# Optimization experiments

Hardware: AMD Instinct MI355X
Metric: run time of the kernel (lower is better)

The kernel has to match this reference:

```python
import jax, jax.numpy as jnp
import numpy as np

VAR0, VAR1 = 0.1, 0.2      # cfg['variance']
THR = 0.5                   # overlap_thresh
NEGPOS_RATIO = 3


def point_form(p):  # center form [P,4] -> corner form
    return jnp.concatenate([p[:, :2] - p[:, 2:] / 2, p[:, :2] + p[:, 2:] / 2], axis=1)


def iou(a, b):  # a [N,4], b [P,4], both corner form -> [N,P]
    lt = jnp.maximum(a[:, None, :2], b[None, :, :2])
    rb = jnp.minimum(a[:, None, 2:], b[None, :, 2:])
    wh = jnp.maximum(rb - lt, 0.0)
    inter = wh[..., 0] * wh[..., 1]
    area_a = (a[:, 2] - a[:, 0]) * (a[:, 3] - a[:, 1])
    area_b = (b[:, 2] - b[:, 0]) * (b[:, 3] - b[:, 1])
    return inter / (area_a[:, None] + area_b[None, :] - inter)


def encode(matched, priors):  # matched corner [P,4], priors center [P,4]
    g_cxcy = ((matched[:, :2] + matched[:, 2:]) / 2 - priors[:, :2]) / (VAR0 * priors[:, 2:])
    g_wh = jnp.log((matched[:, 2:] - matched[:, :2]) / priors[:, 2:]) / VAR1
    return jnp.concatenate([g_cxcy, g_wh], axis=1)


def match_one(truths, labels, priors):
    # truths [N,4] corner, labels [N] int, priors [P,4] center
    ov = iou(truths, point_form(priors))            # [N,P]
    best_prior_idx = jnp.argmax(ov, axis=1)         # [N] best prior per truth
    best_truth_overlap = jnp.max(ov, axis=0)        # [P]
    best_truth_idx = jnp.argmax(ov, axis=0)         # [P]
    # ensure every truth keeps its best prior
    best_truth_overlap = best_truth_overlap.at[best_prior_idx].set(2.0)
    best_truth_idx = best_truth_idx.at[best_prior_idx].set(jnp.arange(truths.shape[0]))
    matched = truths[best_truth_idx]                # [P,4]
    conf = jnp.where(best_truth_overlap < THR, 0, labels[best_truth_idx] + 1)  # bkg=0
    return encode(matched, priors), conf


def multibox_loss(loc_data, conf_data, priors, truths, labels):
    B, P, C = conf_data.shape
    loc_t, conf_t = jax.vmap(lambda t, l: match_one(t, l, priors))(truths, labels)
    loc_t = jax.lax.stop_gradient(loc_t)            # targets are detached
    pos = conf_t > 0                                # [B,P]

    # localization: masked smooth-L1 (beta=1), sum reduction
    d = loc_data - loc_t
    ad = jnp.abs(d)
    sl1 = jnp.where(ad < 1.0, 0.5 * d * d, ad - 0.5)
    loss_l = jnp.sum(sl1 * pos[..., None].astype(sl1.dtype))

    # hard negative mining: per-prior CE proxy, positives zeroed, double argsort rank
    lse = jax.nn.logsumexp(conf_data, axis=2)
    gathered = jnp.take_along_axis(conf_data, conf_t[..., None], axis=2)[..., 0]
    lc = jnp.where(pos, 0.0, lse - gathered)        # [B,P]
    loss_idx = jnp.argsort(-lc, axis=1)
    idx_rank = jnp.argsort(loss_idx, axis=1)
    num_pos = jnp.sum(pos, axis=1)                  # [B]
    num_neg = jnp.minimum(NEGPOS_RATIO * num_pos, P - 1)
    neg = idx_rank < num_neg[:, None]
    sel = pos | neg

    # confidence loss on pos + hard negatives, sum reduction
    logp = jax.nn.log_softmax(conf_data, axis=2)
    ce = -jnp.take_along_axis(logp, conf_t[..., None], axis=2)[..., 0]
    loss_c = jnp.sum(ce * sel.astype(ce.dtype))

    total = jnp.sum(num_pos).astype(loss_l.dtype)
    return loss_l / total, loss_c / total


def setup_inputs() -> dict:
    key = jax.random.key(0)
    kl, kc, kp, kt, ky = jax.random.split(key, 5)
    B, P, C, N = 64, 24564, 21, 16
    loc_data = 0.1 * jax.random.normal(kl, (B, P, 4), dtype=jnp.float32)
    conf_data = jax.random.normal(kc, (B, P, C), dtype=jnp.float32)
    pr = jax.random.uniform(kp, (P, 4), dtype=jnp.float32)
    priors = jnp.concatenate([pr[:, :2] * 0.9 + 0.05, pr[:, 2:] * 0.26 + 0.04], axis=1)
    pts = jax.random.uniform(kt, (B, N, 2, 2), dtype=jnp.float32) * 0.8 + 0.05
    truths = jnp.concatenate([jnp.min(pts, axis=2), jnp.max(pts, axis=2) + 0.02], axis=-1)
    labels = jax.random.randint(ky, (B, N), 0, 20, dtype=jnp.int32)
    return {"loc_data": loc_data, "conf_data": conf_data, "priors": priors,
            "truths": truths, "labels": labels}


def reference(loc_data, conf_data, priors, truths, labels):
    return multibox_loss(loc_data, conf_data, priors, truths, labels)
```

## Files before the change

kernel.cpp:

```cpp
#include <hip/hip_runtime.h>
#include <math.h>

constexpr int Bn = 64;
constexpr int Pn = 24564;
constexpr int Cn = 21;
constexpr int Nn = 16;
constexpr int CH = 12;
constexpr int CHSZ = 2048;
constexpr float VAR0 = 0.1f, VAR1 = 0.2f, THRv = 0.5f;

__device__ __forceinline__ float iou_tp(float tx1, float ty1, float tx2, float ty2,
                                        float px1, float py1, float px2, float py2) {
  float lx = fmaxf(tx1, px1), ly = fmaxf(ty1, py1);
  float rx = fminf(tx2, px2), ry = fminf(ty2, py2);
  float w = fmaxf(rx - lx, 0.f), h = fmaxf(ry - ly, 0.f);
  float inter = w * h;
  float aa = (tx2 - tx1) * (ty2 - ty1);
  float ab = (px2 - px1) * (py2 - py1);
  return __fdividef(inter, aa + ab - inter);
}

__global__ void best_prior_part(const float* __restrict__ priors,
                                const float* __restrict__ truths,
                                float* __restrict__ pbv, int* __restrict__ pbi) {
  const int c = blockIdx.x;
  const int b = blockIdx.y;
  const int tid = threadIdx.x;
  __shared__ float4 tru[Nn];
  if (tid < Nn) tru[tid] = reinterpret_cast<const float4*>(truths)[b * Nn + tid];
  __syncthreads();

  float bv[Nn];
  int bi[Nn];
#pragma unroll
  for (int n = 0; n < Nn; n++) { bv[n] = -1.0f; bi[n] = 0x7fffffff; }

  const int base = c * CHSZ;
#pragma unroll
  for (int j = 0; j < CHSZ / 256; j++) {
    int p = base + j * 256 + tid;
    if (p < Pn) {
      float4 pr = reinterpret_cast<const float4*>(priors)[p];
      float px1 = pr.x - pr.z * 0.5f, py1 = pr.y - pr.w * 0.5f;
      float px2 = pr.x + pr.z * 0.5f, py2 = pr.y + pr.w * 0.5f;
#pragma unroll
      for (int n = 0; n < Nn; n++) {
        float v = iou_tp(tru[n].x, tru[n].y, tru[n].z, tru[n].w, px1, py1, px2, py2);
        if (v > bv[n]) { bv[n] = v; bi[n] = p; }
      }
    }
  }

  const int lane = tid & 63, wv = tid >> 6;
  __shared__ float swv[4][Nn];
  __shared__ int swi[4][Nn];
#pragma unroll
  for (int n = 0; n < Nn; n++) {
    float v = bv[n]; int i = bi[n];
#pragma unroll
    for (int m = 1; m < 64; m <<= 1) {
      float ov = __shfl_xor(v, m, 64);
      int oi = __shfl_xor(i, m, 64);
      if (ov > v || (ov == v && oi < i)) { v = ov; i = oi; }
    }
    if (lane == 0) { swv[wv][n] = v; swi[wv][n] = i; }
  }
  __syncthreads();
  if (tid < Nn) {
    float v = swv[0][tid]; int i = swi[0][tid];
#pragma unroll
    for (int w = 1; w < 4; w++) {
      float ov = swv[w][tid]; int oi = swi[w][tid];
      if (ov > v || (ov == v && oi < i)) { v = ov; i = oi; }
    }
    pbv[(b * CH + c) * Nn + tid] = v;
    pbi[(b * CH + c) * Nn + tid] = i;
  }
}

__global__ void best_prior_merge(const float* __restrict__ pbv,
                                 const int* __restrict__ pbi,
                                 int* __restrict__ bpi) {
  const int b = blockIdx.x;
  const int n = threadIdx.x;
  if (n < Nn) {
    float v = pbv[(b * CH) * Nn + n];
    int i = pbi[(b * CH) * Nn + n];
#pragma unroll
    for (int c = 1; c < CH; c++) {
      float ov = pbv[(b * CH + c) * Nn + n];
      int oi = pbi[(b * CH + c) * Nn + n];
      if (ov > v || (ov == v && oi < i)) { v = ov; i = oi; }
    }
    bpi[b * Nn + n] = i;
  }
}

__global__ __launch_bounds__(256, 8) void match_loss_kernel(
    const float* __restrict__ loc,
    const float* __restrict__ conf,
    const float* __restrict__ priors,
    const float* __restrict__ truths,
    const int* __restrict__ labels,
    const int* __restrict__ bpi,
    float* __restrict__ lc_out,
    int* __restrict__ num_pos,
    float* __restrict__ acc ) {
  const int b = blockIdx.y;
  const int tid = threadIdx.x;
  const int wv = tid >> 6, lane = tid & 63;
  const int p = blockIdx.x * 256 + tid;

  __shared__ float4 tru[Nn];
  __shared__ int lab[Nn];
  __shared__ int bp[Nn];
  if (tid < Nn) {
    tru[tid] = reinterpret_cast<const float4*>(truths)[b * Nn + tid];
    lab[tid] = labels[b * Nn + tid];
    bp[tid]  = bpi[b * Nn + tid];
  }
  __syncthreads();

  float my_ll = 0.f, my_cep = 0.f;
  int my_np = 0;

  if (p < Pn) {
    const float* crow = conf + ((size_t)b * Pn + p) * Cn;
    float r[Cn];
#pragma unroll
    for (int c = 0; c < Cn; c++) r[c] = crow[c];

    float4 pr = reinterpret_cast<const float4*>(priors)[p];
    float px1 = pr.x - pr.z * 0.5f, py1 = pr.y - pr.w * 0.5f;
    float px2 = pr.x + pr.z * 0.5f, py2 = pr.y + pr.w * 0.5f;

    float best = -1.0f;
    int bidx = 0;
#pragma unroll
    for (int n = 0; n < Nn; n++) {
      float v = iou_tp(tru[n].x, tru[n].y, tru[n].z, tru[n].w, px1, py1, px2, py2);
      if (v > best) { best = v; bidx = n; }
    }
#pragma unroll
    for (int n = 0; n < Nn; n++) {
      if (bp[n] == p) { best = 2.0f; bidx = n; }
    }

    int conf_t = (best < THRv) ? 0 : (lab[bidx] + 1);
    bool pos = conf_t > 0;

    float s = 0.f;
#pragma unroll
    for (int c = 0; c < Cn; c++) s += __expf(r[c]);
    float lse = __logf(s);
    float ce = lse - crow[conf_t];

    lc_out[(size_t)b * Pn + p] = pos ? 0.f : ce;

    if (pos) {
      my_np = 1;
      my_cep = ce;
      float4 t = tru[bidx];
      float gx = ((t.x + t.z) * 0.5f - pr.x) / (VAR0 * pr.z);
      float gy = ((t.y + t.w) * 0.5f - pr.y) / (VAR0 * pr.w);
      float gw = __logf((t.z - t.x) / pr.z) / VAR1;
      float gh = __logf((t.w - t.y) / pr.w) / VAR1;
      const float* lrow = loc + ((size_t)b * Pn + p) * 4;
      float d0 = lrow[0] - gx, d1 = lrow[1] - gy, d2 = lrow[2] - gw, d3 = lrow[3] - gh;
      float a0 = fabsf(d0), a1 = fabsf(d1), a2 = fabsf(d2), a3 = fabsf(d3);
      my_ll  = (a0 < 1.f ? 0.5f * d0 * d0 : a0 - 0.5f);
      my_ll += (a1 < 1.f ? 0.5f * d1 * d1 : a1 - 0.5f);
      my_ll += (a2 < 1.f ? 0.5f * d2 * d2 : a2 - 0.5f);
      my_ll += (a3 < 1.f ? 0.5f * d3 * d3 : a3 - 0.5f);
    }
  }

  float ll = my_ll, cep = my_cep;
  int np = my_np;
#pragma unroll
  for (int m2 = 1; m2 < 64; m2 <<= 1) {
    ll  += __shfl_xor(ll, m2, 64);
    cep += __shfl_xor(cep, m2, 64);
    np  += __shfl_xor(np, m2, 64);
  }
  __shared__ float sw_ll[4], sw_ce[4];
  __shared__ int sw_np[4];
  if (lane == 0) { sw_ll[wv] = ll; sw_ce[wv] = cep; sw_np[wv] = np; }
  __syncthreads();
  if (tid == 0) {
    float tll = sw_ll[0] + sw_ll[1] + sw_ll[2] + sw_ll[3];
    float tce = sw_ce[0] + sw_ce[1] + sw_ce[2] + sw_ce[3];
    int tnp = sw_np[0] + sw_np[1] + sw_np[2] + sw_np[3];
    if (tll != 0.f) atomicAdd(&acc[0], tll);
    if (tce != 0.f) atomicAdd(&acc[1], tce);
    if (tnp != 0)   atomicAdd(&num_pos[b], tnp);
  }
}

__global__ __launch_bounds__(1024) void topk_kernel(const float* __restrict__ lc,
                                                    const int* __restrict__ num_pos,
                                                    float* __restrict__ topk) {
  const int b = blockIdx.x;
  const int tid = threadIdx.x;
  const int wv = tid >> 6, lane = tid & 63;
  const float* row = lc + (size_t)b * Pn;
  const int K = min(3 * num_pos[b], Pn - 1);

  __shared__ unsigned cnt[16][256];
  __shared__ float bsum[16][256];
  __shared__ unsigned mcnt[256];
  __shared__ float msum[256];
  __shared__ unsigned sh_prefix;
  __shared__ int sh_rem;
  __shared__ float sh_sum;
  __shared__ int sh_done;
  if (tid == 0) { sh_prefix = 0u; sh_rem = K; sh_sum = 0.f; sh_done = (K <= 0) ? 1 : 0; }
  __syncthreads();

  for (int pass = 0; pass < 4; pass++) {
    if (sh_done) break;
    const int shift = 24 - pass * 8;
    for (int q = lane; q < 256; q += 64) { cnt[wv][q] = 0u; bsum[wv][q] = 0.f; }
    __syncthreads();
    const unsigned pref = sh_prefix;
    for (int p = tid; p < Pn; p += 1024) {
      float f = row[p];
      unsigned u = __float_as_uint(f) | 0x80000000u;
      bool match = (pass == 0) || ((u >> (32 - 8 * pass)) == pref);
      if (match) {
        unsigned bkt = (u >> shift) & 255u;
        atomicAdd(&cnt[wv][bkt], 1u);
        atomicAdd(&bsum[wv][bkt], f);
      }
    }
    __syncthreads();
    if (tid < 256) {
      unsigned ctot = 0; float stot = 0.f;
#pragma unroll
      for (int w = 0; w < 16; w++) { ctot += cnt[w][tid]; stot += bsum[w][tid]; }
      mcnt[tid] = ctot; msum[tid] = stot;
    }
    __syncthreads();
    if (tid == 0) {
      int rem = sh_rem;
      float ssum = sh_sum;
      unsigned pivot = 0u;
      int done = 0;
      for (int bkt = 255; bkt >= 0; bkt--) {
        unsigned cb = mcnt[bkt];
        if ((int)cb <= rem) {
          ssum += msum[bkt];
          rem -= (int)cb;
          if (rem == 0) { done = 1; break; }
        } else {
          pivot = (unsigned)bkt;
          break;
        }
      }
      if (!done && pass == 3) {
        unsigned key = (sh_prefix << 8) | pivot;
        float f = __uint_as_float(key & 0x7fffffffu);
        ssum += (float)rem * f;
        done = 1;
      }
      sh_prefix = (sh_prefix << 8) | pivot;
      sh_rem = rem;
      sh_sum = ssum;
      sh_done = done;
    }
    __syncthreads();
  }
  if (tid == 0) topk[b] = sh_sum;
}

__global__ void finalize_kernel(const int* __restrict__ num_pos,
                                const float* __restrict__ topk,
                                const float* __restrict__ acc,
                                float* __restrict__ out) {
  const int t = threadIdx.x;
  int np = num_pos[t];
  float tk = topk[t];
#pragma unroll
  for (int m = 1; m < 64; m <<= 1) {
    np += __shfl_xor(np, m, 64);
    tk += __shfl_xor(tk, m, 64);
  }
  if (t == 0) {
    float ftot = (float)np;
    out[0] = acc[0] / ftot;
    out[1] = (acc[1] + tk) / ftot;
  }
}

extern "C" void kernel_launch(void* const* d_in, const int* in_sizes, int n_in,
                              void* d_out, int out_size, void* d_ws, size_t ws_size,
                              hipStream_t stream) {
  const float* loc    = (const float*)d_in[0];
  const float* conf   = (const float*)d_in[1];
  const float* priors = (const float*)d_in[2];
  const float* truths = (const float*)d_in[3];
  const int*   labels = (const int*)d_in[4];
  float* out = (float*)d_out;

  float* lc      = (float*)d_ws;
  int*   num_pos = (int*)(lc + (size_t)Bn * Pn);
  float* topk    = (float*)(num_pos + Bn);
  float* acc     = topk + Bn;
  int*   bpi     = (int*)(acc + 2);
  float* pbv     = (float*)(bpi + Bn * Nn);
  int*   pbi     = (int*)(pbv + Bn * CH * Nn);

  size_t zbytes = (size_t)(Bn + Bn + 2 + Bn * Nn) * 4;
  hipMemsetAsync(num_pos, 0, zbytes, stream);

  dim3 gridA(CH, Bn);
  best_prior_part<<<gridA, 256, 0, stream>>>(priors, truths, pbv, pbi);
  best_prior_merge<<<Bn, 64, 0, stream>>>(pbv, pbi, bpi);

  dim3 gridB((Pn + 255) / 256, Bn);
  match_loss_kernel<<<gridB, 256, 0, stream>>>(loc, conf, priors, truths, labels, bpi,
                                               lc, num_pos, acc);

  topk_kernel<<<Bn, 1024, 0, stream>>>(lc, num_pos, topk);

  finalize_kernel<<<1, 64, 0, stream>>>(num_pos, topk, acc, out);
}
```

Before: 500.5 us.

## Split conf log-sum-exp into coalesced wave-per-row-group kernel

Moves the cross-entropy/log-sum-exp computation out of the matching kernel into a separate kernel. In the new kernel each wave processes three 21-class rows at a time with lane-contiguous loads and a shuffle reduction, replacing the old pattern where each thread loaded its own strided 21-float row. The matching kernel now writes conf_t to a new workspace buffer, which the new kernel reads. This trades an extra launch and an extra int buffer round trip for coalesced access to the large conf tensor, though 1 of every 64 lanes sits idle.

```diff
diff --git a/kernel.cpp b/kernel.cpp
--- a/kernel.cpp
+++ b/kernel.cpp
@@ -8,6 +8,7 @@
 constexpr int CH = 12;
 constexpr int CHSZ = 2048;
 constexpr float VAR0 = 0.1f, VAR1 = 0.2f, THRv = 0.5f;
+constexpr int ROWS = Bn * Pn;
 
 __device__ __forceinline__ float iou_tp(float tx1, float ty1, float tx2, float ty2,
                                         float px1, float py1, float px2, float py2) {
@@ -96,14 +97,13 @@
   }
 }
 
-__global__ __launch_bounds__(256, 8) void match_loss_kernel(
+__global__ __launch_bounds__(256) void match_kernel(
     const float* __restrict__ loc,
-    const float* __restrict__ conf,
     const float* __restrict__ priors,
     const float* __restrict__ truths,
     const int* __restrict__ labels,
     const int* __restrict__ bpi,
-    float* __restrict__ lc_out,
+    int* __restrict__ conf_t_out,
     int* __restrict__ num_pos,
     float* __restrict__ acc ) {
   const int b = blockIdx.y;
@@ -121,15 +121,10 @@
   }
   __syncthreads();
 
-  float my_ll = 0.f, my_cep = 0.f;
+  float my_ll = 0.f;
   int my_np = 0;
 
   if (p < Pn) {
-    const float* crow = conf + ((size_t)b * Pn + p) * Cn;
-    float r[Cn];
-#pragma unroll
-    for (int c = 0; c < Cn; c++) r[c] = crow[c];
-
     float4 pr = reinterpret_cast<const float4*>(priors)[p];
     float px1 = pr.x - pr.z * 0.5f, py1 = pr.y - pr.w * 0.5f;
     float px2 = pr.x + pr.z * 0.5f, py2 = pr.y + pr.w * 0.5f;
@@ -147,19 +142,10 @@
     }
 
     int conf_t = (best < THRv) ? 0 : (lab[bidx] + 1);
-    bool pos = conf_t > 0;
-
-    float s = 0.f;
-#pragma unroll
-    for (int c = 0; c < Cn; c++) s += __expf(r[c]);
-    float lse = __logf(s);
-    float ce = lse - crow[conf_t];
-
-    lc_out[(size_t)b * Pn + p] = pos ? 0.f : ce;
-
-    if (pos) {
+    conf_t_out[(size_t)b * Pn + p] = conf_t;
+
+    if (conf_t > 0) {
       my_np = 1;
-      my_cep = ce;
       float4 t = tru[bidx];
       float gx = ((t.x + t.z) * 0.5f - pr.x) / (VAR0 * pr.z);
       float gy = ((t.y + t.w) * 0.5f - pr.y) / (VAR0 * pr.w);
@@ -175,25 +161,81 @@
     }
   }
 
-  float ll = my_ll, cep = my_cep;
+  float ll = my_ll;
   int np = my_np;
 #pragma unroll
   for (int m2 = 1; m2 < 64; m2 <<= 1) {
-    ll  += __shfl_xor(ll, m2, 64);
-    cep += __shfl_xor(cep, m2, 64);
-    np  += __shfl_xor(np, m2, 64);
-  }
-  __shared__ float sw_ll[4], sw_ce[4];
+    ll += __shfl_xor(ll, m2, 64);
+    np += __shfl_xor(np, m2, 64);
+  }
+  __shared__ float sw_ll[4];
   __shared__ int sw_np[4];
-  if (lane == 0) { sw_ll[wv] = ll; sw_ce[wv] = cep; sw_np[wv] = np; }
+  if (lane == 0) { sw_ll[wv] = ll; sw_np[wv] = np; }
   __syncthreads();
   if (tid == 0) {
     float tll = sw_ll[0] + sw_ll[1] + sw_ll[2] + sw_ll[3];
-    float tce = sw_ce[0] + sw_ce[1] + sw_ce[2] + sw_ce[3];
     int tnp = sw_np[0] + sw_np[1] + sw_np[2] + sw_np[3];
     if (tll != 0.f) atomicAdd(&acc[0], tll);
-    if (tce != 0.f) atomicAdd(&acc[1], tce);
     if (tnp != 0)   atomicAdd(&num_pos[b], tnp);
+  }
+}
+
+constexpr int B2_BLOCKS = 2048;
+constexpr int B2_WAVES = B2_BLOCKS * 4;
+constexpr int B2_CHUNK = (ROWS + B2_WAVES - 1) / B2_WAVES;
+
+__global__ __launch_bounds__(256) void lse_kernel(
+    const float* __restrict__ conf,
+    const int* __restrict__ conf_t,
+    float* __restrict__ lc_out,
+    float* __restrict__ acc ) {
+  const int tid = threadIdx.x;
+  const int lane = tid & 63;
+  const int gwave = (blockIdx.x * 256 + tid) >> 6;
+  const int row_off = lane / 21;
+  const int cls = lane - row_off * 21;
+  const bool lane_ok = (row_off < 3);
+
+  const int r_begin = gwave * B2_CHUNK;
+  const int r_end   = min(r_begin + B2_CHUNK, ROWS);
+
+  float my_cep = 0.f;
+
+  for (int r0 = r_begin; r0 < r_end; r0 += 3) {
+    const int row = r0 + row_off;
+    const bool valid = lane_ok && (row < ROWS);
+    float x = 0.f;
+    int ct = 0;
+    if (valid) {
+      x = conf[(size_t)r0 * Cn + lane];
+      ct = conf_t[row];
+    }
+    float e = valid ? __expf(x) : 0.f;
+    float g = (valid && cls == ct) ? x : 0.f;
+#pragma unroll
+    for (int off = 16; off > 0; off >>= 1) {
+      float e2 = __shfl_down(e, off, 64);
+      float g2 = __shfl_down(g, off, 64);
+      if (cls + off < 21) { e += e2; g += g2; }
+    }
+    if (valid && cls == 0) {
+      float ce = __logf(e) - g;
+      bool pos = ct > 0;
+      lc_out[row] = pos ? 0.f : ce;
+      if (pos) my_cep += ce;
+    }
+  }
+
+  float cep = my_cep;
+#pragma unroll
+  for (int m2 = 1; m2 < 64; m2 <<= 1) cep += __shfl_xor(cep, m2, 64);
+  __shared__ float sw_ce[4];
+  const int wv = tid >> 6;
+  if (lane == 0) sw_ce[wv] = cep;
+  __syncthreads();
+  if (tid == 0) {
+    float t = sw_ce[0] + sw_ce[1] + sw_ce[2] + sw_ce[3];
+    if (t != 0.f) atomicAdd(&acc[1], t);
   }
 }
 
@@ -303,7 +345,8 @@
   float* out = (float*)d_out;
 
   float* lc      = (float*)d_ws;
-  int*   num_pos = (int*)(lc + (size_t)Bn * Pn);
+  int*   ctbuf   = (int*)(lc + (size_t)Bn * Pn);
+  int*   num_pos = ctbuf + (size_t)Bn * Pn;
   float* topk    = (float*)(num_pos + Bn);
   float* acc     = topk + Bn;
   int*   bpi     = (int*)(acc + 2);
@@ -318,8 +361,10 @@
   best_prior_merge<<<Bn, 64, 0, stream>>>(pbv, pbi, bpi);
 
   dim3 gridB((Pn + 255) / 256, Bn);
-  match_loss_kernel<<<gridB, 256, 0, stream>>>(loc, conf, priors, truths, labels, bpi,
-                                               lc, num_pos, acc);
+  match_kernel<<<gridB, 256, 0, stream>>>(loc, priors, truths, labels, bpi,
+                                          ctbuf, num_pos, acc);
+
+  lse_kernel<<<B2_BLOCKS, 256, 0, stream>>>(conf, ctbuf, lc, acc);
 
   topk_kernel<<<Bn, 1024, 0, stream>>>(lc, num_pos, topk);
 
```

Measured after the change: 512.2 us. 1.02x slower.
